# Optimization experiments

Measured on AMD Instinct MI355X. Metric: run time of the kernel, lower is better.

The kernel has to match this reference:

```python
import jax, jax.numpy as jnp
import numpy as np

NUM_OBJ = 32
OBJ_DIM = 128
MSG_W = 256
FIN_W = 256
BATCH = 256
BN_EPS = 1e-5
NEG_SLOPE = 0.01


def _linear_init(key, fan_in, fan_out):
    # torch nn.Linear default: U(-1/sqrt(fan_in), 1/sqrt(fan_in))
    kw, kb = jax.random.split(key)
    bound = 1.0 / np.sqrt(fan_in)
    w = jax.random.uniform(kw, (fan_out, fan_in), jnp.float32, -bound, bound)
    b = jax.random.uniform(kb, (fan_out,), jnp.float32, -bound, bound)
    return w, b


def setup_inputs() -> dict:
    key = jax.random.key(0)
    ks = jax.random.split(key, 8)
    state = jax.random.normal(ks[0], (BATCH, NUM_OBJ, OBJ_DIM), jnp.float32)
    edges = jax.random.randint(ks[1], (BATCH, NUM_OBJ * NUM_OBJ), 0, 2).astype(jnp.float32)
    msg_w1, msg_b1 = _linear_init(ks[2], OBJ_DIM * 2, MSG_W)
    msg_w2, msg_b2 = _linear_init(ks[3], MSG_W, OBJ_DIM)
    fin_w1, fin_b1 = _linear_init(ks[4], OBJ_DIM * 2, FIN_W)
    fin_w2, fin_b2 = _linear_init(ks[5], FIN_W, OBJ_DIM)
    msg_gamma = jnp.ones((MSG_W,), jnp.float32)
    msg_beta = jnp.zeros((MSG_W,), jnp.float32)
    fin_gamma = jnp.ones((FIN_W,), jnp.float32)
    fin_beta = jnp.zeros((FIN_W,), jnp.float32)
    return {
        "state": state, "edges": edges,
        "msg_w1": msg_w1, "msg_b1": msg_b1, "msg_gamma": msg_gamma, "msg_beta": msg_beta,
        "msg_w2": msg_w2, "msg_b2": msg_b2,
        "fin_w1": fin_w1, "fin_b1": fin_b1, "fin_gamma": fin_gamma, "fin_beta": fin_beta,
        "fin_w2": fin_w2, "fin_b2": fin_b2,
    }


def _batchnorm_train(x, gamma, beta):
    # training-mode BatchNorm1d: batch stats over rows, biased variance
    mean = jnp.mean(x, axis=0)
    var = jnp.mean(jnp.square(x - mean), axis=0)
    return (x - mean) * jax.lax.rsqrt(var + BN_EPS) * gamma + beta


def _mlp(x, w1, b1, gamma, beta, w2, b2):
    h = x @ w1.T + b1
    h = _batchnorm_train(h, gamma, beta)
    h = jnp.where(h >= 0, h, NEG_SLOPE * h)  # LeakyReLU
    return h @ w2.T + b2


def reference(state, edges, msg_w1, msg_b1, msg_gamma, msg_beta, msg_w2, msg_b2,
              fin_w1, fin_b1, fin_gamma, fin_beta, fin_w2, fin_b2):
    B, n, d = state.shape
    src = jnp.repeat(jnp.arange(n), n)   # [n*n]
    tgt = jnp.tile(jnp.arange(n), n)     # [n*n]
    sources = state[:, src]              # [B, n*n, d]
    targets = state[:, tgt]              # [B, n*n, d]
    e = edges[:, :, None]                # [B, n*n, 1]
    need = jnp.concatenate([sources * e, targets * e], axis=2)  # [B, n*n, 2d]
    msgs = _mlp(need.reshape(-1, 2 * d), msg_w1, msg_b1, msg_gamma, msg_beta, msg_w2, msg_b2)
    agg = jnp.sum(msgs.reshape(B, n, n, d), axis=2)  # sum over inner edge group
    sm = jnp.concatenate([state, agg], axis=2).reshape(-1, 2 * d)
    out = _mlp(sm, fin_w1, fin_b1, fin_gamma, fin_beta, fin_w2, fin_b2)
    return out.reshape(B, n, d)
```

## Files before the change

kernel.cpp:

```cpp
#include <hip/hip_runtime.h>

#define NPAIR  262144
#define BN_EPS 1e-5f

typedef unsigned short u16;
typedef unsigned int   u32;
typedef __attribute__((ext_vector_type(8))) short bf16x8;
typedef __attribute__((ext_vector_type(4))) float f32x4;
typedef __attribute__((ext_vector_type(4))) unsigned short u16x4;
typedef __attribute__((ext_vector_type(4))) unsigned int u32x4;

__device__ __forceinline__ u16 f2bf(float f) {
    union { float f; unsigned u; } v; v.f = f;
    unsigned r = v.u + 0x7fffu + ((v.u >> 16) & 1u);
    return (u16)(r >> 16);
}
__device__ __forceinline__ float bf2f(u16 u) {
    union { unsigned u; float f; } v; v.u = ((unsigned)u) << 16; return v.f;
}
__device__ __forceinline__ bf16x8 cvt8_f32(const float* p) {
    f32x4 v0 = *(const f32x4*)p, v1 = *(const f32x4*)(p + 4);
    bf16x8 r;
    #pragma unroll
    for (int k = 0; k < 4; ++k) {
        r[k]     = (short)f2bf(v0[k]);
        r[4 + k] = (short)f2bf(v1[k]);
    }
    return r;
}
__device__ __forceinline__ bf16x8 cvt8_bn_b(const u16* p, const float* a, const float* d) {
    u16x4 v0 = *(const u16x4*)p, v1 = *(const u16x4*)(p + 4);
    f32x4 a0 = *(const f32x4*)a, a1 = *(const f32x4*)(a + 4);
    f32x4 d0 = *(const f32x4*)d, d1 = *(const f32x4*)(d + 4);
    bf16x8 r;
    #pragma unroll
    for (int k = 0; k < 4; ++k) {
        float x0 = fmaf(a0[k], bf2f(v0[k]), d0[k]); x0 = fmaxf(x0, 0.01f * x0);
        float x1 = fmaf(a1[k], bf2f(v1[k]), d1[k]); x1 = fmaxf(x1, 0.01f * x1);
        r[k]     = (short)f2bf(x0);
        r[4 + k] = (short)f2bf(x1);
    }
    return r;
}

__global__ __launch_bounds__(1024) void pq_stats(
    const float* __restrict__ state, const float* __restrict__ w1,
    const float* __restrict__ edges, const float* __restrict__ b1,
    u16* __restrict__ PQb, float* __restrict__ EQf,
    float* __restrict__ sums)
{
    __shared__ float Qls[33 * 256];
    __shared__ float redA[16 * 256];
    __shared__ float redB[16 * 256];
    __shared__ u32 masks[32];
    __shared__ __align__(16) unsigned char list8[32 * 32];
    __shared__ float cdf[32];

    const int b    = blockIdx.x;
    const int t    = threadIdx.x;
    const int lane = t & 63;
    const int w    = t >> 6;
    const int lr   = lane & 15;
    const int lk   = (lane >> 4) * 8;
    const int c0   = lane * 4;

    if (t < 256) ((u32*)list8)[t] = 0x20202020u;
    if (t < 64) { const f32x4 z = {}; *(f32x4*)&Qls[32 * 256 + t * 4] = z; }

    const float ev = edges[(size_t)b * 1024 + t];

    const int col0 = w * 32;
    f32x4 acc[2][2] = {};
    #pragma unroll
    for (int ks = 0; ks < 4; ++ks) {
        const int kabs = ks * 32 + lk;
        bf16x8 af[2];
        #pragma unroll
        for (int rf = 0; rf < 2; ++rf)
            af[rf] = cvt8_f32(state + (size_t)(b * 32 + rf * 16 + lr) * 128 + kabs);
        #pragma unroll
        for (int cf = 0; cf < 2; ++cf) {
            const int coln = col0 + cf * 16 + lr;
            const float* wp = (coln < 256) ? (w1 + (size_t)coln * 256 + kabs)
                                           : (w1 + (size_t)(coln - 256) * 256 + 128 + kabs);
            const bf16x8 bfr = cvt8_f32(wp);
            #pragma unroll
            for (int rf = 0; rf < 2; ++rf)
                acc[rf][cf] = __builtin_amdgcn_mfma_f32_16x16x32_bf16(af[rf], bfr, acc[rf][cf], 0, 0, 0);
        }
    }
    #pragma unroll
    for (int rf = 0; rf < 2; ++rf)
        #pragma unroll
        for (int cf = 0; cf < 2; ++cf) {
            const int col = col0 + cf * 16 + lr;
            #pragma unroll
            for (int r = 0; r < 4; ++r) {
                const int row = rf * 16 + (lane >> 4) * 4 + r;
                const u16 u = f2bf(acc[rf][cf][r]);
                PQb[(size_t)(b * 32 + row) * 512 + col] = u;
                if (col >= 256) Qls[row * 256 + (col - 256)] = bf2f(u);
            }
        }
    __syncthreads();

    {
        const int il_t = t >> 5;
        const int j_t  = t & 31;
        const unsigned long long bal = __ballot(ev != 0.f);
        const u32 m32 = (lane < 32) ? (u32)bal : (u32)(bal >> 32);
        if (ev != 0.f)
            list8[il_t * 32 + __popc(m32 & ((1u << j_t) - 1u))] = (unsigned char)j_t;
        if (j_t == 0) masks[il_t] = m32;
    }
    __syncthreads();

    if (t < 32) {
        u32 cnt = 0;
        #pragma unroll
        for (int i = 0; i < 32; ++i) cnt += (masks[i] >> t) & 1u;
        cdf[t] = (float)cnt;
    }
    if (t == 0) {
        int tot = 0;
        #pragma unroll
        for (int i = 0; i < 32; ++i) tot += __popc(masks[i]);
        atomicAdd(&sums[512], (float)tot);
    }

    const f32x4 b14 = *(const f32x4*)(b1 + c0);
    f32x4 sumA = {}, sumB = {};

    #pragma unroll
    for (int ii = 0; ii < 2; ++ii) {
        const int il = 2 * w + ii;
        const int n1 = __popc(masks[il]);
        const int npad = (n1 + 3) & ~3;
        const float frd = (float)n1;
        f32x4 eq = {};
        const u32x4 l0 = *(const u32x4*)(list8 + il * 32);
        const u32x4 l1 = *(const u32x4*)(list8 + il * 32 + 16);
        const u32 wbuf[8] = {l0[0], l0[1], l0[2], l0[3], l1[0], l1[1], l1[2], l1[3]};
        #pragma unroll
        for (int wi = 0; wi < 8; ++wi) {
            if (wi * 4 >= npad) break;
            const u32 w4 = wbuf[wi];
            #pragma unroll
            for (int kb = 0; kb < 4; ++kb) {
                const int j = (w4 >> (kb * 8)) & 0xff;
                const f32x4 q = *(const f32x4*)&Qls[j * 256 + c0];
                #pragma unroll
                for (int k = 0; k < 4; ++k) eq[k] += q[k];
            }
        }
        *(f32x4*)(EQf + (size_t)(b * 32 + il) * 256 + c0) = eq;
        const u16x4 pu = *(const u16x4*)(PQb + (size_t)(b * 32 + il) * 512 + c0);
        #pragma unroll
        for (int k = 0; k < 4; ++k) {
            const float pb = bf2f(pu[k]) + b14[k];
            sumA[k] += frd * pb + eq[k];
            sumB[k] = fmaf(frd * pb + 2.f * eq[k], pb, sumB[k]);
        }
    }
    __syncthreads();

    #pragma unroll
    for (int jj = 0; jj < 2; ++jj) {
        const int j = 2 * w + jj;
        const float cdj = cdf[j];
        const f32x4 q = *(const f32x4*)&Qls[j * 256 + c0];
        #pragma unroll
        for (int k = 0; k < 4; ++k) sumB[k] = fmaf(cdj * q[k], q[k], sumB[k]);
    }
    *(f32x4*)&redA[w * 256 + c0] = sumA;
    *(f32x4*)&redB[w * 256 + c0] = sumB;
    __syncthreads();
    if (t < 256) {
        float a = 0.f, bb = 0.f;
        #pragma unroll
        for (int ww = 0; ww < 16; ++ww) {
            a  += redA[ww * 256 + t];
            bb += redB[ww * 256 + t];
        }
        atomicAdd(&sums[t], a);
        atomicAdd(&sums[256 + t], bb);
    }
}

__global__ __launch_bounds__(512) void s_agg_h2_kernel(
    const u16* __restrict__ PQb, const float* __restrict__ edges,
    const float* __restrict__ EQf, const float* __restrict__ sums,
    const float* __restrict__ gamma, const float* __restrict__ beta,
    const float* __restrict__ b1, const float* __restrict__ state,
    const float* __restrict__ w2, const float* __restrict__ b2,
    const float* __restrict__ fw1, const float* __restrict__ fb1,
    u16* __restrict__ H2b, float* __restrict__ sums2)
{
    __shared__ float Qls[33 * 256];
    __shared__ u16 Ssb[16 * 256];
    __shared__ u16 Asb[16 * 128];
    __shared__ u16 aggs[16 * 128];
    __shared__ __align__(16) unsigned char list8[16 * 32];
    __shared__ int n1s[16];
    __shared__ float sred[512];

    const int b    = blockIdx.x;
    const int i0   = blockIdx.y * 16;
    const int t    = threadIdx.x;
    const int lane = t & 63;
    const int w    = t >> 6;
    const int lr   = lane & 15;
    const int lkg  = lane >> 4;
    const int lk   = lkg * 8;
    const int c0   = lane * 4;

    sred[t] = 0.f;

    const float Etot = sums[512];
    const float nz   = (float)NPAIR - Etot;
    const float invN = 1.f / (float)NPAIR;
    const f32x4 s1  = *(const f32x4*)(sums + c0);
    const f32x4 s2  = *(const f32x4*)(sums + 256 + c0);
    const f32x4 g4  = *(const f32x4*)(gamma + c0);
    const f32x4 be4 = *(const f32x4*)(beta + c0);
    const f32x4 b14 = *(const f32x4*)(b1 + c0);
    f32x4 a4, d4, ld4;
    #pragma unroll
    for (int k = 0; k < 4; ++k) {
        const float mean = (s1[k] + nz * b14[k]) * invN;
        const float ms   = (s2[k] + nz * b14[k] * b14[k]) * invN;
        const float var  = fmaf(-mean, mean, ms);
        a4[k]  = g4[k] * rsqrtf(var + BN_EPS);
        d4[k]  = fmaf(b14[k] - mean, a4[k], be4[k]);
        ld4[k] = fmaxf(d4[k], 0.01f * d4[k]);
    }

    #pragma unroll
    for (int it = 0; it < 4; ++it) {
        const int row = w + it * 8;
        const u16x4 qu = *(const u16x4*)(PQb + (size_t)(b * 32 + row) * 512 + 256 + c0);
        f32x4 q;
        #pragma unroll
        for (int k = 0; k < 4; ++k) q[k] = a4[k] * bf2f(qu[k]);
        *(f32x4*)&Qls[row * 256 + c0] = q;
    }
    if (t < 256) {
        const int row = t >> 4, k8 = (t & 15) * 8;
        const bf16x8 av = cvt8_f32(state + (size_t)(b * 32 + i0 + row) * 128 + k8);
        *(bf16x8*)((char*)Asb + ((row * 256 + k8 * 2) ^ ((row & 7) << 4))) = av;
    }
    if (t < 64) { const f32x4 z = {}; *(f32x4*)&Qls[32 * 256 + t * 4] = z; }
    if (t < 128) ((u32*)list8)[t] = 0x20202020u;

    const float ev = edges[(size_t)b * 1024 + (i0 + (t >> 5)) * 32 + (t & 31)];
    __syncthreads();

    {
        const int il_t = t >> 5;
        const int j_t  = t & 31;
        const unsigned long long bal = __ballot(ev != 0.f);
        const u32 m32 = (lane < 32) ? (u32)bal : (u32)(bal >> 32);
        if (ev != 0.f)
            list8[il_t * 32 + __popc(m32 & ((1u << j_t) - 1u))] = (unsigned char)j_t;
        if (j_t == 0) n1s[il_t] = __popc(m32);
    }
    __syncthreads();

    #pragma unroll
    for (int ii = 0; ii < 2; ++ii) {
        const int il = 2 * w + ii;
        const int gi = b * 32 + i0 + il;
        const int n1 = n1s[il];
        const int npad = (n1 + 3) & ~3;
        const float frd = (float)n1;
        const float fz = (float)(32 - n1);
        const float fp = (float)(npad - n1);
        const u16x4 pu = *(const u16x4*)(PQb + (size_t)gi * 512 + c0);
        const f32x4 eq4 = *(const f32x4*)(EQf + (size_t)gi * 256 + c0);
        f32x4 ap, absacc;
        #pragma unroll
        for (int k = 0; k < 4; ++k) {
            ap[k] = fmaf(a4[k], bf2f(pu[k]), d4[k]);
            absacc[k] = -fp * fabsf(ap[k]);
        }
        const u32x4 l0 = *(const u32x4*)(list8 + il * 32);
        const u32x4 l1 = *(const u32x4*)(list8 + il * 32 + 16);
        const u32 wbuf[8] = {l0[0], l0[1], l0[2], l0[3], l1[0], l1[1], l1[2], l1[3]};
        #pragma unroll
        for (int wi = 0; wi < 8; ++wi) {
            if (wi * 4 >= npad) break;
            const u32 w4 = wbuf[wi];
            #pragma unroll
            for (int kb = 0; kb < 4; ++kb) {
                const int j = (w4 >> (kb * 8)) & 0xff;
                const f32x4 q = *(const f32x4*)&Qls[j * 256 + c0];
                #pragma unroll
                for (int k = 0; k < 4; ++k)
                    absacc[k] += fabsf(ap[k] + q[k]);
            }
        }
        u16x4 o;
        #pragma unroll
        for (int k = 0; k < 4; ++k) {
            const float lin = fmaf(frd, ap[k], a4[k] * eq4[k]);
            const float S = fmaf(fz, ld4[k], fmaf(0.505f, lin, 0.495f * absacc[k]));
            o[k] = f2bf(S);
        }
        *(u16x4*)((char*)Ssb + il * 512 + ((lane * 8) ^ ((il & 7) << 4))) = o;
    }
    __syncthreads();

    {
        f32x4 acc2 = {};
        #pragma unroll
        for (int ks = 0; ks < 8; ++ks) {
            const int rdoff = (ks * 64 + lkg * 16) ^ ((lr & 7) << 4);
            const bf16x8 afr = *(const bf16x8*)((const char*)Ssb + lr * 512 + rdoff);
            const bf16x8 bfr = cvt8_f32(w2 + (size_t)(w * 16 + lr) * 256 + ks * 32 + lk);
            acc2 = __builtin_amdgcn_mfma_f32_16x16x32_bf16(afr, bfr, acc2, 0, 0, 0);
        }
        const int col = w * 16 + lr;
        const float bv = 32.f * b2[col];
        #pragma unroll
        for (int r = 0; r < 4; ++r) {
            const int row = lkg * 4 + r;
            *(u16*)((char*)aggs + ((row * 256 + col * 2) ^ ((row & 7) << 4))) = f2bf(acc2[r] + bv);
        }
    }
    __syncthreads();

    {
        f32x4 acc3[2] = {};
        #pragma unroll
        for (int ks = 0; ks < 8; ++ks) {
            const int kabs = ks * 32 + lk;
            const int row = lr;
            bf16x8 af3;
            if (ks < 4)
                af3 = *(const bf16x8*)((const char*)Asb + ((row * 256 + kabs * 2) ^ ((row & 7) << 4)));
            else
                af3 = *(const bf16x8*)((const char*)aggs + ((row * 256 + (kabs - 128) * 2) ^ ((row & 7) << 4)));
            #pragma unroll
            for (int cf = 0; cf < 2; ++cf) {
                const int col = w * 32 + cf * 16 + lr;
                const bf16x8 bfr = cvt8_f32(fw1 + (size_t)col * 256 + kabs);
                acc3[cf] = __builtin_amdgcn_mfma_f32_16x16x32_bf16(af3, bfr, acc3[cf], 0, 0, 0);
            }
        }
        #pragma unroll
        for (int cf = 0; cf < 2; ++cf) {
            const int col = w * 32 + cf * 16 + lr;
            const float bv = fb1[col];
            float s = 0.f, ss = 0.f;
            #pragma unroll
            for (int r = 0; r < 4; ++r) {
                const int row = lkg * 4 + r;
                const float v = acc3[cf][r] + bv;
                H2b[(size_t)(b * 32 + i0 + row) * 256 + col] = f2bf(v);
                s += v;
                ss = fmaf(v, v, ss);
            }
            atomicAdd(&sred[col], s);
            atomicAdd(&sred[256 + col], ss);
        }
    }
    __syncthreads();
    if (t < 256) {
        atomicAdd(&sums2[t], sred[t]);
        atomicAdd(&sums2[256 + t], sred[256 + t]);
    }
}

__global__ __launch_bounds__(256) void out_gemm(
    const u16* __restrict__ H2b, const float* __restrict__ fw2,
    const float* __restrict__ fb2, const float* __restrict__ sums2,
    const float* __restrict__ gamma, const float* __restrict__ beta,
    float* __restrict__ out)
{
    __shared__ float adl[512];
    const int t = threadIdx.x;
    {
        const float invR = 1.f / 8192.f;
        const float mean = sums2[t] * invR;
        const float var  = fmaf(-mean, mean, sums2[256 + t] * invR);
        const float a    = gamma[t] * rsqrtf(var + BN_EPS);
        adl[t]       = a;
        adl[256 + t] = fmaf(-mean, a, beta[t]);
    }
    __syncthreads();

    const int lane = t & 63;
    const int wave = t >> 6;
    const int row0 = blockIdx.y * 64 + wave * 16;
    const int col0 = blockIdx.x * 32;
    const int lr = lane & 15;
    const int lk = (lane >> 4) * 8;

    f32x4 acc[2] = {};
    #pragma unroll
    for (int ks = 0; ks < 8; ++ks) {
        const int kabs = ks * 32 + lk;
        const bf16x8 af = cvt8_bn_b(H2b + (size_t)(row0 + lr) * 256 + kabs,
                                    adl + kabs, adl + 256 + kabs);
        #pragma unroll
        for (int cf = 0; cf < 2; ++cf) {
            const bf16x8 bf = cvt8_f32(fw2 + (size_t)(col0 + cf * 16 + lr) * 256 + kabs);
            acc[cf] = __builtin_amdgcn_mfma_f32_16x16x32_bf16(af, bf, acc[cf], 0, 0, 0);
        }
    }
    #pragma unroll
    for (int cf = 0; cf < 2; ++cf) {
        const int col = col0 + cf * 16 + lr;
        const float bv = fb2[col];
        #pragma unroll
        for (int r = 0; r < 4; ++r) {
            const int row = row0 + (lane >> 4) * 4 + r;
            out[(size_t)row * 128 + col] = acc[cf][r] + bv;
        }
    }
}

extern "C" void kernel_launch(void* const* d_in, const int* in_sizes, int n_in,
                              void* d_out, int out_size, void* d_ws, size_t ws_size,
                              hipStream_t stream)
{
    const float* state     = (const float*)d_in[0];
    const float* edges     = (const float*)d_in[1];
    const float* msg_w1    = (const float*)d_in[2];
    const float* msg_b1    = (const float*)d_in[3];
    const float* msg_gamma = (const float*)d_in[4];
    const float* msg_beta  = (const float*)d_in[5];
    const float* msg_w2    = (const float*)d_in[6];
    const float* msg_b2    = (const float*)d_in[7];
    const float* fin_w1    = (const float*)d_in[8];
    const float* fin_b1    = (const float*)d_in[9];
    const float* fin_gamma = (const float*)d_in[10];
    const float* fin_beta  = (const float*)d_in[11];
    const float* fin_w2    = (const float*)d_in[12];
    const float* fin_b2    = (const float*)d_in[13];

    char* w = (char*)d_ws;
    u16*   PQb  = (u16*)(w);
    float* EQf  = (float*)(w + 8388608);
    u16*   H2b  = (u16*)(w + 16777216);
    float* sums = (float*)(w + 20971520);
    float* sums2 = sums + 544;

    hipMemsetAsync(sums, 0, 1088 * sizeof(float), stream);

    pq_stats<<<256, 1024, 0, stream>>>(state, msg_w1, edges, msg_b1,
                                       PQb, EQf, sums);

    s_agg_h2_kernel<<<dim3(256, 2), 512, 0, stream>>>(
        PQb, edges, EQf, sums, msg_gamma, msg_beta, msg_b1,
        state, msg_w2, msg_b2, fin_w1, fin_b1, H2b, sums2);

    out_gemm<<<dim3(4, 128), 256, 0, stream>>>(
        H2b, fin_w2, fin_b2, sums2, fin_gamma, fin_beta, (float*)d_out);
}
```

Baseline: 82.93 us.

## Pre-convert weights to bf16 once and recompute edge Q sums instead of storing

A new prep kernel converts all four weight matrices to bf16 once and zeroes the stats buffers, replacing the memset. The GEMM kernels then load bf16 weights directly instead of converting fp32 weights in every block. The EQ buffer (8 MB) is no longer written in pq_stats and read back in s_agg_h2; the linear Q sum is instead accumulated inside the existing gather loop. This adds one small kernel launch in exchange for less global traffic and less conversion work.

```diff
diff --git a/kernel.cpp b/kernel.cpp
--- a/kernel.cpp
+++ b/kernel.cpp
@@ -18,6 +18,11 @@
 __device__ __forceinline__ float bf2f(u16 u) {
     union { unsigned u; float f; } v; v.u = ((unsigned)u) << 16; return v.f;
 }
+__device__ __forceinline__ u16x4 cvt4(float4 v) {
+    u16x4 r;
+    r[0] = f2bf(v.x); r[1] = f2bf(v.y); r[2] = f2bf(v.z); r[3] = f2bf(v.w);
+    return r;
+}
 __device__ __forceinline__ bf16x8 cvt8_f32(const float* p) {
     f32x4 v0 = *(const f32x4*)p, v1 = *(const f32x4*)(p + 4);
     bf16x8 r;
@@ -43,11 +48,34 @@
     return r;
 }
 
+__global__ __launch_bounds__(256) void prep_kernel(
+    const float* __restrict__ w1, const float4* __restrict__ w2,
+    const float4* __restrict__ fw1, const float4* __restrict__ fw2,
+    u16x4* __restrict__ W1b, u16x4* __restrict__ W2b,
+    u16x4* __restrict__ FW1b, u16x4* __restrict__ FW2b,
+    f32x4* __restrict__ sums)
+{
+    int g = blockIdx.x * 256 + threadIdx.x;
+    if (g < 16384) {
+        const int o = g * 4, n = o >> 7, k = o & 127;
+        const float4 v = *(const float4*)(w1 + (n < 256 ? n * 256 + k
+                                                        : (n - 256) * 256 + 128 + k));
+        W1b[g] = cvt4(v); return;
+    }
+    g -= 16384;
+    if (g < 8192) { W2b[g] = cvt4(w2[g]); return; }
+    g -= 8192;
+    if (g < 16384) { FW1b[g] = cvt4(fw1[g]); return; }
+    g -= 16384;
+    if (g < 8192) { FW2b[g] = cvt4(fw2[g]); return; }
+    g -= 8192;
+    if (g < 264) { const f32x4 z = {}; sums[g] = z; }
+}
+
 __global__ __launch_bounds__(1024) void pq_stats(
-    const float* __restrict__ state, const float* __restrict__ w1,
+    const float* __restrict__ state, const u16* __restrict__ W1b,
     const float* __restrict__ edges, const float* __restrict__ b1,
-    u16* __restrict__ PQb, float* __restrict__ EQf,
-    float* __restrict__ sums)
+    u16* __restrict__ PQb, float* __restrict__ sums)
 {
     __shared__ float Qls[33 * 256];
     __shared__ float redA[16 * 256];
@@ -80,10 +108,7 @@
             af[rf] = cvt8_f32(state + (size_t)(b * 32 + rf * 16 + lr) * 128 + kabs);
         #pragma unroll
         for (int cf = 0; cf < 2; ++cf) {
-            const int coln = col0 + cf * 16 + lr;
-            const float* wp = (coln < 256) ? (w1 + (size_t)coln * 256 + kabs)
-                                           : (w1 + (size_t)(coln - 256) * 256 + 128 + kabs);
-            const bf16x8 bfr = cvt8_f32(wp);
+            const bf16x8 bfr = *(const bf16x8*)(W1b + (size_t)(col0 + cf * 16 + lr) * 128 + kabs);
             #pragma unroll
             for (int rf = 0; rf < 2; ++rf)
                 acc[rf][cf] = __builtin_amdgcn_mfma_f32_16x16x32_bf16(af[rf], bfr, acc[rf][cf], 0, 0, 0);
@@ -153,7 +178,6 @@
                 for (int k = 0; k < 4; ++k) eq[k] += q[k];
             }
         }
-        *(f32x4*)(EQf + (size_t)(b * 32 + il) * 256 + c0) = eq;
         const u16x4 pu = *(const u16x4*)(PQb + (size_t)(b * 32 + il) * 512 + c0);
         #pragma unroll
         for (int k = 0; k < 4; ++k) {
@@ -189,11 +213,11 @@
 
 __global__ __launch_bounds__(512) void s_agg_h2_kernel(
     const u16* __restrict__ PQb, const float* __restrict__ edges,
-    const float* __restrict__ EQf, const float* __restrict__ sums,
-    const float* __restrict__ gamma, const float* __restrict__ beta,
-    const float* __restrict__ b1, const float* __restrict__ state,
-    const float* __restrict__ w2, const float* __restrict__ b2,
-    const float* __restrict__ fw1, const float* __restrict__ fb1,
+    const float* __restrict__ sums, const float* __restrict__ gamma,
+    const float* __restrict__ beta, const float* __restrict__ b1,
+    const float* __restrict__ state,
+    const u16* __restrict__ W2b, const float* __restrict__ b2,
+    const u16* __restrict__ FW1b, const float* __restrict__ fb1,
     u16* __restrict__ H2b, float* __restrict__ sums2)
 {
     __shared__ float Qls[33 * 256];
@@ -276,8 +300,7 @@
         const float fz = (float)(32 - n1);
         const float fp = (float)(npad - n1);
         const u16x4 pu = *(const u16x4*)(PQb + (size_t)gi * 512 + c0);
-        const f32x4 eq4 = *(const f32x4*)(EQf + (size_t)gi * 256 + c0);
-        f32x4 ap, absacc;
+        f32x4 ap, absacc, linq = {};
         #pragma unroll
         for (int k = 0; k < 4; ++k) {
             ap[k] = fmaf(a4[k], bf2f(pu[k]), d4[k]);
@@ -295,14 +318,16 @@
                 const int j = (w4 >> (kb * 8)) & 0xff;
                 const f32x4 q = *(const f32x4*)&Qls[j * 256 + c0];
                 #pragma unroll
-                for (int k = 0; k < 4; ++k)
+                for (int k = 0; k < 4; ++k) {
                     absacc[k] += fabsf(ap[k] + q[k]);
+                    linq[k]   += q[k];
+                }
             }
         }
         u16x4 o;
         #pragma unroll
         for (int k = 0; k < 4; ++k) {
-            const float lin = fmaf(frd, ap[k], a4[k] * eq4[k]);
+            const float lin = fmaf(frd, ap[k], linq[k]);
             const float S = fmaf(fz, ld4[k], fmaf(0.505f, lin, 0.495f * absacc[k]));
             o[k] = f2bf(S);
         }
@@ -316,7 +341,7 @@
         for (int ks = 0; ks < 8; ++ks) {
             const int rdoff = (ks * 64 + lkg * 16) ^ ((lr & 7) << 4);
             const bf16x8 afr = *(const bf16x8*)((const char*)Ssb + lr * 512 + rdoff);
-            const bf16x8 bfr = cvt8_f32(w2 + (size_t)(w * 16 + lr) * 256 + ks * 32 + lk);
+            const bf16x8 bfr = *(const bf16x8*)(W2b + (size_t)(w * 16 + lr) * 256 + ks * 32 + lk);
             acc2 = __builtin_amdgcn_mfma_f32_16x16x32_bf16(afr, bfr, acc2, 0, 0, 0);
         }
         const int col = w * 16 + lr;
@@ -343,7 +368,7 @@
             #pragma unroll
             for (int cf = 0; cf < 2; ++cf) {
                 const int col = w * 32 + cf * 16 + lr;
-                const bf16x8 bfr = cvt8_f32(fw1 + (size_t)col * 256 + kabs);
+                const bf16x8 bfr = *(const bf16x8*)(FW1b + (size_t)col * 256 + kabs);
                 acc3[cf] = __builtin_amdgcn_mfma_f32_16x16x32_bf16(af3, bfr, acc3[cf], 0, 0, 0);
             }
         }
@@ -372,7 +397,7 @@
 }
 
 __global__ __launch_bounds__(256) void out_gemm(
-    const u16* __restrict__ H2b, const float* __restrict__ fw2,
+    const u16* __restrict__ H2b, const u16* __restrict__ FW2b,
     const float* __restrict__ fb2, const float* __restrict__ sums2,
     const float* __restrict__ gamma, const float* __restrict__ beta,
     float* __restrict__ out)
@@ -404,7 +429,7 @@
                                     adl + kabs, adl + 256 + kabs);
         #pragma unroll
         for (int cf = 0; cf < 2; ++cf) {
-            const bf16x8 bf = cvt8_f32(fw2 + (size_t)(col0 + cf * 16 + lr) * 256 + kabs);
+            const bf16x8 bf = *(const bf16x8*)(FW2b + (size_t)(col0 + cf * 16 + lr) * 256 + kabs);
             acc[cf] = __builtin_amdgcn_mfma_f32_16x16x32_bf16(af, bf, acc[cf], 0, 0, 0);
         }
     }
@@ -441,20 +466,24 @@
 
     char* w = (char*)d_ws;
     u16*   PQb  = (u16*)(w);
-    float* EQf  = (float*)(w + 8388608);
-    u16*   H2b  = (u16*)(w + 16777216);
-    float* sums = (float*)(w + 20971520);
+    u16*   H2b  = (u16*)(w + 8388608);
+    u16*   W1b  = (u16*)(w + 12582912);
+    u16*   W2b  = (u16*)(w + 12713984);
+    u16*   FW1b = (u16*)(w + 12779520);
+    u16*   FW2b = (u16*)(w + 12910592);
+    float* sums = (float*)(w + 12976128);
     float* sums2 = sums + 544;
 
-    hipMemsetAsync(sums, 0, 1088 * sizeof(float), stream);
-
-    pq_stats<<<256, 1024, 0, stream>>>(state, msg_w1, edges, msg_b1,
-                                       PQb, EQf, sums);
+    prep_kernel<<<194, 256, 0, stream>>>(
+        msg_w1, (const float4*)msg_w2, (const float4*)fin_w1, (const float4*)fin_w2,
+        (u16x4*)W1b, (u16x4*)W2b, (u16x4*)FW1b, (u16x4*)FW2b, (f32x4*)sums);
+
+    pq_stats<<<256, 1024, 0, stream>>>(state, W1b, edges, msg_b1, PQb, sums);
 
     s_agg_h2_kernel<<<dim3(256, 2), 512, 0, stream>>>(
-        PQb, edges, EQf, sums, msg_gamma, msg_beta, msg_b1,
-        state, msg_w2, msg_b2, fin_w1, fin_b1, H2b, sums2);
+        PQb, edges, sums, msg_gamma, msg_beta, msg_b1,
+        state, W2b, msg_b2, FW1b, fin_b1, H2b, sums2);
 
     out_gemm<<<dim3(4, 128), 256, 0, stream>>>(
-        H2b, fin_w2, fin_b2, sums2, fin_gamma, fin_beta, (float*)d_out);
-}
+        H2b, FW2b, fin_b2, sums2, fin_gamma, fin_beta, (float*)d_out);
+}
```

New measurement: 67.00 us (median of 4 runs). 19.2% less time.
